# Kernel optimization log

Hardware: AMD Instinct MI355X
Metric: run time of the kernel (lower is better)

## Reference

```python
import jax, jax.numpy as jnp
import numpy as np

B, N, C = 2, 384, 128
D = C // 4          # bottleneck_dim
H = 128             # time_mlp_hidden_dim


def setup_inputs() -> dict:
    key = jax.random.key(0)
    ks = jax.random.split(key, 12)
    s = 0.02
    return {
        "edge_embed": jax.random.normal(ks[0], (B, N, N, C), jnp.float32),
        "edge_mask": jax.random.randint(ks[1], (B, N, N), 0, 2, jnp.int32),
        "r3_t": jax.random.uniform(ks[2], (B,), jnp.float32),
        # linear params stored as [in, out]
        "Wg": jax.random.normal(ks[3], (C, D), jnp.float32) * s,
        "bg": jnp.zeros((D,), jnp.float32),
        "Wv": jax.random.normal(ks[4], (C, D), jnp.float32) * s,
        "bv": jnp.zeros((D,), jnp.float32),
        "Wd": jax.random.normal(ks[5], (C, D), jnp.float32) * s,
        "bd": jnp.zeros((D,), jnp.float32),
        "Wo": jax.random.normal(ks[6], (D, C), jnp.float32) * s,
        "bo": jnp.zeros((C,), jnp.float32),
        "W1": jax.random.normal(ks[7], (1, H), jnp.float32) * s,
        "b1": jnp.zeros((H,), jnp.float32),
        "W2": jax.random.normal(ks[8], (H, 2 * C), jnp.float32) * s,
        "b2": jnp.zeros((2 * C,), jnp.float32),
    }


def reference(edge_embed, edge_mask, r3_t, Wg, bg, Wv, bv, Wd, bd, Wo, bo, W1, b1, W2, b2):
    Bb, Nn, _, Cc = edge_embed.shape
    P = edge_embed.reshape(Bb, Nn * Nn, Cc)          # [B, N^2, C]
    m = (edge_mask.reshape(Bb, Nn * Nn, 1) != 0)
    mf = m.astype(P.dtype)

    fP = P @ Wg + bg                                 # [B, N^2, D]
    gP = P @ Wv + bv                                 # [B, N^2, D]
    fP = jnp.where(m, fP, jnp.asarray(-1e8, P.dtype))
    w = jax.nn.softmax(fP, axis=1)                   # softmax over all edges
    w = w * mf
    w = w / (w.sum(axis=1, keepdims=True) + 1e-8)

    V = jnp.einsum('bnd,bne->bde', w, gP)            # [B, D, D] global context

    hP = jax.nn.softmax(P @ Wd + bd, axis=2)         # softmax over channels
    O = jnp.einsum('bnd,bde->bne', hP, V)            # redistribute
    O = (O @ Wo + bo).reshape(Bb, Nn, Nn, Cc)

    # FiLM conditioned on timestep (torch GELU is exact erf form)
    t = r3_t.reshape(Bb, 1)
    t_emb = jax.nn.gelu(t @ W1 + b1, approximate=False) @ W2 + b2
    scale, shift = jnp.split(t_emb, 2, axis=-1)
    O = O * (1 + scale[:, None, None, :]) + shift[:, None, None, :]

    return edge_embed + O
```

## Files before the change

kernel.cpp:

```cpp
#include <hip/hip_runtime.h>
#include <hip/hip_bf16.h>
#include <math.h>

#define N2 147456
#define CC 128
#define TILES 2304

#define WS_VACC 0
#define WS_S    2048
#define WS_UP   2112
#define WS_B2   10304

typedef __attribute__((ext_vector_type(8))) __bf16 bf16x8;
typedef __attribute__((ext_vector_type(4))) __bf16 bf16x4;
typedef __attribute__((ext_vector_type(4))) float f32x4;

#define MFMA16(a_, b_, c_) __builtin_amdgcn_mfma_f32_16x16x32_bf16((a_), (b_), (c_), 0, 0, 0)

__global__ void k0_zero(float* __restrict__ ws) {
    int i = blockIdx.x * 256 + threadIdx.x;
    if (i < 2112) ws[i] = 0.0f;
}

__global__ __launch_bounds__(256, 3) void k1_accum(
    const float* __restrict__ P, const int* __restrict__ mask,
    const float* __restrict__ Wg, const float* __restrict__ bg,
    const float* __restrict__ Wv, const float* __restrict__ bv,
    float* __restrict__ ws)
{
    __shared__ __bf16 ef_t[32][72];
    __shared__ __bf16 gv_t[32][72];

    const int t  = threadIdx.x;
    const int b  = blockIdx.y;
    const int w  = t >> 6;
    const int l  = t & 63;
    const int lr = l & 15;
    const int lg = l >> 4;

    bf16x8 wfrag[2][2][4];
    #pragma unroll
    for (int nt = 0; nt < 2; ++nt)
      #pragma unroll
      for (int ks = 0; ks < 4; ++ks) {
        const int base = (ks * 32 + 8 * lg) * 32 + nt * 16 + lr;
        bf16x8 f0, f1;
        #pragma unroll
        for (int i = 0; i < 8; ++i) {
            f0[i] = (__bf16)Wg[base + i * 32];
            f1[i] = (__bf16)Wv[base + i * 32];
        }
        wfrag[0][nt][ks] = f0;
        wfrag[1][nt][ks] = f1;
      }
    const float bgv[2] = { bg[lr], bg[lr + 16] };
    const float bvv[2] = { bv[lr], bv[lr + 16] };

    const int mt = w >> 1, ntq = w & 1;
    f32x4 vacc = {0.f, 0.f, 0.f, 0.f};
    float accS = 0.f;
    const int sd = t >> 3, ss = t & 7;

    const float* Pb = P + (size_t)b * N2 * CC;
    const int*   mb = mask + (size_t)b * N2;

    for (int tile = blockIdx.x; tile < TILES; tile += gridDim.x) {
        const int row0 = tile * 64 + w * 16;
        const float* prow = Pb + (size_t)(row0 + lr) * CC + 8 * lg;

        bf16x8 afrag[4];
        #pragma unroll
        for (int ks = 0; ks < 4; ++ks) {
            const float4 a0 = *(const float4*)(prow + ks * 32);
            const float4 a1 = *(const float4*)(prow + ks * 32 + 4);
            bf16x8 f;
            f[0] = (__bf16)a0.x; f[1] = (__bf16)a0.y; f[2] = (__bf16)a0.z; f[3] = (__bf16)a0.w;
            f[4] = (__bf16)a1.x; f[5] = (__bf16)a1.y; f[6] = (__bf16)a1.z; f[7] = (__bf16)a1.w;
            afrag[ks] = f;
        }

        f32x4 facc0 = {0,0,0,0}, facc1 = {0,0,0,0}, gacc0 = {0,0,0,0}, gacc1 = {0,0,0,0};
        #pragma unroll
        for (int ks = 0; ks < 4; ++ks) {
            facc0 = MFMA16(afrag[ks], wfrag[0][0][ks], facc0);
            facc1 = MFMA16(afrag[ks], wfrag[0][1][ks], facc1);
            gacc0 = MFMA16(afrag[ks], wfrag[1][0][ks], gacc0);
            gacc1 = MFMA16(afrag[ks], wfrag[1][1][ks], gacc1);
        }

        int mk[4];
        #pragma unroll
        for (int r = 0; r < 4; ++r) mk[r] = mb[row0 + lg * 4 + r];

        bf16x4 pe0, pe1, pg0, pg1;
        #pragma unroll
        for (int r = 0; r < 4; ++r) {
            pe0[r] = (__bf16)(mk[r] ? __expf(facc0[r] + bgv[0]) : 0.0f);
            pe1[r] = (__bf16)(mk[r] ? __expf(facc1[r] + bgv[1]) : 0.0f);
            pg0[r] = (__bf16)(gacc0[r] + bvv[0]);
            pg1[r] = (__bf16)(gacc1[r] + bvv[1]);
        }
        const int cbase = w * 16 + lg * 4;
        *(bf16x4*)&ef_t[lr     ][cbase] = pe0;
        *(bf16x4*)&ef_t[lr + 16][cbase] = pe1;
        *(bf16x4*)&gv_t[lr     ][cbase] = pg0;
        *(bf16x4*)&gv_t[lr + 16][cbase] = pg1;
        __syncthreads();

        #pragma unroll
        for (int ks = 0; ks < 2; ++ks) {
            const bf16x8 ea = *(const bf16x8*)&ef_t[mt  * 16 + lr][ks * 32 + 8 * lg];
            const bf16x8 gb = *(const bf16x8*)&gv_t[ntq * 16 + lr][ks * 32 + 8 * lg];
            vacc = MFMA16(ea, gb, vacc);
        }
        {
            const bf16x8 ev = *(const bf16x8*)&ef_t[sd][ss * 8];
            float s = 0.f;
            #pragma unroll
            for (int i = 0; i < 8; ++i) s += (float)ev[i];
            accS += s;
        }
        __syncthreads();
    }

    #pragma unroll
    for (int r = 0; r < 4; ++r) {
        const int d = mt * 16 + lg * 4 + r;
        const int e = ntq * 16 + lr;
        atomicAdd(ws + WS_VACC + b * 1024 + d * 32 + e, vacc[r]);
    }
    accS += __shfl_xor(accS, 1);
    accS += __shfl_xor(accS, 2);
    accS += __shfl_xor(accS, 4);
    if (ss == 0) atomicAdd(ws + WS_S + b * 32 + sd, accS);
}

__global__ __launch_bounds__(1024) void k2_finalize(
    const float* __restrict__ r3t,
    const float* __restrict__ Wo, const float* __restrict__ bo,
    const float* __restrict__ W1, const float* __restrict__ b1,
    const float* __restrict__ W2, const float* __restrict__ b2,
    float* __restrict__ ws)
{
    __shared__ float h_lds[2][128];
    __shared__ float fs_lds[2][128];
    __shared__ float sh_lds[2][128];
    __shared__ float V_lds[2048];
    __shared__ float wo_lds[32][128];
    const int t = threadIdx.x;

    ((float4*)&wo_lds[0][0])[t] = ((const float4*)Wo)[t];

    if (t < 256) {
        const int b = t >> 7, j = t & 127;
        const float x = r3t[b] * W1[j] + b1[j];
        h_lds[b][j] = 0.5f * x * (1.0f + erff(x * 0.7071067811865475f));
    }
    __syncthreads();

    if (t < 512) {
        const int b = t >> 8, j2 = t & 255;
        float acc = b2[j2];
        for (int k = 0; k < 128; ++k) acc += h_lds[b][k] * W2[k * 256 + j2];
        if (j2 < 128) fs_lds[b][j2] = 1.0f + acc;
        else          sh_lds[b][j2 - 128] = acc;
    }
    #pragma unroll
    for (int i = 0; i < 2; ++i) {
        const int idx = t + i * 1024;
        const int b = idx >> 10, d = (idx >> 5) & 31;
        const float s = ws[WS_S + b * 32 + d];
        V_lds[idx] = ws[WS_VACC + idx] / (s * (1.0f + 1e-8f));
    }
    __syncthreads();

    if (t < 256) {
        const int b = t >> 7, c = t & 127;
        ws[WS_B2 + t] = bo[c] * fs_lds[b][c] + sh_lds[b][c];
    }
    #pragma unroll
    for (int i = 0; i < 8; ++i) {
        const int idx = t + i * 1024;
        const int b = idx >> 12, d = (idx >> 7) & 31, c = idx & 127;
        float acc = 0.0f;
        #pragma unroll
        for (int e = 0; e < 32; ++e) acc += V_lds[b * 1024 + d * 32 + e] * wo_lds[e][c];
        ws[WS_UP + idx] = acc * fs_lds[b][c];
    }
}

__global__ __launch_bounds__(256, 3) void k3_out(
    const float* __restrict__ P,
    const float* __restrict__ Wd, const float* __restrict__ bd,
    const float* __restrict__ ws, float* __restrict__ out)
{
    __shared__ float  u_lds[32][132];
    __shared__ __bf16 h_t[64][40];

    const int t  = threadIdx.x;
    const int b  = blockIdx.y;
    const int w  = t >> 6, l = t & 63, lr = l & 15, lg = l >> 4;

    {
        const float4* src = (const float4*)(ws + WS_UP + b * 4096);
        const int d = t >> 3, c0 = (t & 7) * 16;
        #pragma unroll
        for (int j = 0; j < 4; ++j)
            *(float4*)&u_lds[d][c0 + 4 * j] = src[t * 4 + j];
    }

    bf16x8 wdfrag[2][4];
    #pragma unroll
    for (int nt = 0; nt < 2; ++nt)
      #pragma unroll
      for (int ks = 0; ks < 4; ++ks) {
        const int base = (ks * 32 + 8 * lg) * 32 + nt * 16 + lr;
        bf16x8 f;
        #pragma unroll
        for (int i = 0; i < 8; ++i) f[i] = (__bf16)Wd[base + i * 32];
        wdfrag[nt][ks] = f;
      }

    float bdv[8];
    #pragma unroll
    for (int r = 0; r < 4; ++r) {
        bdv[r]     = bd[lg * 4 + r];
        bdv[4 + r] = bd[16 + lg * 4 + r];
    }
    float b2v[8][4];
    #pragma unroll
    for (int nt = 0; nt < 8; ++nt) {
        const float4 v = *(const float4*)(ws + WS_B2 + b * 128 + nt * 16 + lg * 4);
        b2v[nt][0] = v.x; b2v[nt][1] = v.y; b2v[nt][2] = v.z; b2v[nt][3] = v.w;
    }

    __syncthreads();

    bf16x8 ufrag[8];
    #pragma unroll
    for (int nt = 0; nt < 8; ++nt) {
        bf16x8 f;
        #pragma unroll
        for (int i = 0; i < 8; ++i) f[i] = (__bf16)u_lds[8 * lg + i][nt * 16 + lr];
        ufrag[nt] = f;
    }

    const float* Pb = P + (size_t)b * N2 * CC;
    float*       Ob = out + (size_t)b * N2 * CC;

    for (int tile = blockIdx.x; tile < TILES; tile += gridDim.x) {
        const int row0 = tile * 64 + w * 16;
        const float* prow = Pb + (size_t)(row0 + lr) * CC + 8 * lg;

        bf16x8 afrag[4];
        #pragma unroll
        for (int ks = 0; ks < 4; ++ks) {
            const float4 a0 = *(const float4*)(prow + ks * 32);
            const float4 a1 = *(const float4*)(prow + ks * 32 + 4);
            bf16x8 f;
            f[0] = (__bf16)a0.x; f[1] = (__bf16)a0.y; f[2] = (__bf16)a0.z; f[3] = (__bf16)a0.w;
            f[4] = (__bf16)a1.x; f[5] = (__bf16)a1.y; f[6] = (__bf16)a1.z; f[7] = (__bf16)a1.w;
            afrag[ks] = f;
        }

        f32x4 dacc0 = {0,0,0,0}, dacc1 = {0,0,0,0};
        #pragma unroll
        for (int ks = 0; ks < 4; ++ks) {
            dacc0 = MFMA16(wdfrag[0][ks], afrag[ks], dacc0);
            dacc1 = MFMA16(wdfrag[1][ks], afrag[ks], dacc1);
        }

        float v[8];
        #pragma unroll
        for (int r = 0; r < 4; ++r) {
            v[r]     = dacc0[r] + bdv[r];
            v[4 + r] = dacc1[r] + bdv[4 + r];
        }
        float m = v[0];
        #pragma unroll
        for (int j = 1; j < 8; ++j) m = fmaxf(m, v[j]);
        m = fmaxf(m, __shfl_xor(m, 16));
        m = fmaxf(m, __shfl_xor(m, 32));
        float e[8], s = 0.f;
        #pragma unroll
        for (int j = 0; j < 8; ++j) { e[j] = __expf(v[j] - m); s += e[j]; }
        s += __shfl_xor(s, 16);
        s += __shfl_xor(s, 32);
        const float inv = 1.0f / s;

        bf16x4 h0, h1;
        #pragma unroll
        for (int r = 0; r < 4; ++r) {
            h0[r] = (__bf16)(e[r] * inv);
            h1[r] = (__bf16)(e[4 + r] * inv);
        }
        const int hrow = w * 16 + lr;
        *(bf16x4*)&h_t[hrow][lg * 4]      = h0;
        *(bf16x4*)&h_t[hrow][16 + lg * 4] = h1;
        const bf16x8 hf = *(const bf16x8*)&h_t[hrow][8 * lg];

        #pragma unroll
        for (int nt = 0; nt < 8; ++nt) {
            f32x4 ci;
            ci[0] = b2v[nt][0]; ci[1] = b2v[nt][1]; ci[2] = b2v[nt][2]; ci[3] = b2v[nt][3];
            const f32x4 oacc = MFMA16(ufrag[nt], hf, ci);
            const size_t off = (size_t)(row0 + lr) * CC + nt * 16 + lg * 4;
            const float4 p4 = *(const float4*)(Pb + off);
            float4 o4;
            o4.x = p4.x + oacc[0]; o4.y = p4.y + oacc[1];
            o4.z = p4.z + oacc[2]; o4.w = p4.w + oacc[3];
            *(float4*)(Ob + off) = o4;
        }
    }
}

extern "C" void kernel_launch(void* const* d_in, const int* in_sizes, int n_in,
                              void* d_out, int out_size, void* d_ws, size_t ws_size,
                              hipStream_t stream) {
    const float* P   = (const float*)d_in[0];
    const int*   msk = (const int*)d_in[1];
    const float* r3t = (const float*)d_in[2];
    const float* Wg  = (const float*)d_in[3];
    const float* bg  = (const float*)d_in[4];
    const float* Wv  = (const float*)d_in[5];
    const float* bv  = (const float*)d_in[6];
    const float* Wd  = (const float*)d_in[7];
    const float* bd  = (const float*)d_in[8];
    const float* Wo  = (const float*)d_in[9];
    const float* bo  = (const float*)d_in[10];
    const float* W1  = (const float*)d_in[11];
    const float* b1  = (const float*)d_in[12];
    const float* W2  = (const float*)d_in[13];
    const float* b2  = (const float*)d_in[14];
    float* ws  = (float*)d_ws;
    float* out = (float*)d_out;

    hipLaunchKernelGGL(k0_zero,     dim3(9),        dim3(256),  0, stream, ws);
    hipLaunchKernelGGL(k1_accum,    dim3(384, 2),   dim3(256),  0, stream, P, msk, Wg, bg, Wv, bv, ws);
    hipLaunchKernelGGL(k2_finalize, dim3(1),        dim3(1024), 0, stream, r3t, Wo, bo, W1, b1, W2, b2, ws);
    hipLaunchKernelGGL(k3_out,      dim3(768, 2),   dim3(256),  0, stream, P, Wd, bd, ws, out);
}
```

Before: 123.2 us.

## Fuse all four stages into one cooperative kernel with grid syncs

Replaces the four-kernel sequence (zero, accumulate, finalize, output) with a single cooperative launch of 768 blocks that uses grid-wide syncs between phases. Each block recomputes the small finalize step (FiLM MLP, V normalization, V·Wo) redundantly in shared memory instead of relying on a single-block kernel. The aim is to remove launch gaps and the serial one-block finalize stage. In exchange it adds grid-sync overhead, duplicated finalize work per block, and occupancy constraints, since all 768 blocks must be co-resident. It falls back to the old path if the cooperative launch fails.

```diff
diff --git a/kernel.cpp b/kernel.cpp
--- a/kernel.cpp
+++ b/kernel.cpp
@@ -1,10 +1,13 @@
 #include <hip/hip_runtime.h>
+#include <hip/hip_cooperative_groups.h>
 #include <hip/hip_bf16.h>
 #include <math.h>
 
 #define N2 147456
 #define CC 128
 #define TILES 2304
+#define HALFGRID 384
+#define GRID 768
 
 #define WS_VACC 0
 #define WS_S    2048
@@ -16,6 +19,268 @@
 typedef __attribute__((ext_vector_type(4))) float f32x4;
 
 #define MFMA16(a_, b_, c_) __builtin_amdgcn_mfma_f32_16x16x32_bf16((a_), (b_), (c_), 0, 0, 0)
+
+__global__ __launch_bounds__(256, 3) void fused_all(
+    const float* __restrict__ P, const int* __restrict__ mask,
+    const float* __restrict__ r3t,
+    const float* __restrict__ Wg, const float* __restrict__ bg,
+    const float* __restrict__ Wv, const float* __restrict__ bv,
+    const float* __restrict__ Wd, const float* __restrict__ bd,
+    const float* __restrict__ Wo, const float* __restrict__ bo,
+    const float* __restrict__ W1, const float* __restrict__ b1,
+    const float* __restrict__ W2, const float* __restrict__ b2,
+    float* __restrict__ ws, float* __restrict__ out)
+{
+    __shared__ __align__(16) __bf16 ef_t[32][72];
+    __shared__ __align__(16) __bf16 gv_t[32][72];
+    __shared__ __align__(16) float  u_lds[32][132];
+    __shared__ __align__(16) __bf16 h_t[64][40];
+    __shared__ __align__(16) float  fin_V[1024];
+    __shared__ __align__(16) float  fin_h[128];
+    __shared__ __align__(16) float  fin_fs[128];
+    __shared__ __align__(16) float  fin_b2[128];
+
+    const int t  = threadIdx.x;
+    const int bx = blockIdx.x;
+    const int b  = (bx >= HALFGRID) ? 1 : 0;
+    const int tile0 = bx - b * HALFGRID;
+    const int w  = t >> 6;
+    const int l  = t & 63;
+    const int lr = l & 15;
+    const int lg = l >> 4;
+
+    {
+        const int gid = bx * 256 + t;
+        if (gid < 2112) ws[gid] = 0.0f;
+    }
+
+    bf16x8 wfrag[2][2][4];
+    #pragma unroll
+    for (int nt = 0; nt < 2; ++nt)
+      #pragma unroll
+      for (int ks = 0; ks < 4; ++ks) {
+        const int base = (ks * 32 + 8 * lg) * 32 + nt * 16 + lr;
+        bf16x8 f0, f1;
+        #pragma unroll
+        for (int i = 0; i < 8; ++i) {
+            f0[i] = (__bf16)Wg[base + i * 32];
+            f1[i] = (__bf16)Wv[base + i * 32];
+        }
+        wfrag[0][nt][ks] = f0;
+        wfrag[1][nt][ks] = f1;
+      }
+    const float bgv[2] = { bg[lr], bg[lr + 16] };
+    const float bvv[2] = { bv[lr], bv[lr + 16] };
+
+    cooperative_groups::this_grid().sync();
+
+    const float* Pb = P + (size_t)b * N2 * CC;
+
+    {
+        const int* mb = mask + (size_t)b * N2;
+        const int mt = w >> 1, ntq = w & 1;
+        f32x4 vacc = {0.f, 0.f, 0.f, 0.f};
+        float accS = 0.f;
+        const int sd = t >> 3, ss = t & 7;
+
+        for (int tile = tile0; tile < TILES; tile += HALFGRID) {
+            const int row0 = tile * 64 + w * 16;
+            const float* prow = Pb + (size_t)(row0 + lr) * CC + 8 * lg;
+
+            bf16x8 afrag[4];
+            #pragma unroll
+            for (int ks = 0; ks < 4; ++ks) {
+                const float4 a0 = *(const float4*)(prow + ks * 32);
+                const float4 a1 = *(const float4*)(prow + ks * 32 + 4);
+                bf16x8 f;
+                f[0] = (__bf16)a0.x; f[1] = (__bf16)a0.y; f[2] = (__bf16)a0.z; f[3] = (__bf16)a0.w;
+                f[4] = (__bf16)a1.x; f[5] = (__bf16)a1.y; f[6] = (__bf16)a1.z; f[7] = (__bf16)a1.w;
+                afrag[ks] = f;
+            }
+
+            f32x4 facc0 = {0,0,0,0}, facc1 = {0,0,0,0}, gacc0 = {0,0,0,0}, gacc1 = {0,0,0,0};
+            #pragma unroll
+            for (int ks = 0; ks < 4; ++ks) {
+                facc0 = MFMA16(afrag[ks], wfrag[0][0][ks], facc0);
+                facc1 = MFMA16(afrag[ks], wfrag[0][1][ks], facc1);
+                gacc0 = MFMA16(afrag[ks], wfrag[1][0][ks], gacc0);
+                gacc1 = MFMA16(afrag[ks], wfrag[1][1][ks], gacc1);
+            }
+
+            int mk[4];
+            #pragma unroll
+            for (int r = 0; r < 4; ++r) mk[r] = mb[row0 + lg * 4 + r];
+
+            bf16x4 pe0, pe1, pg0, pg1;
+            #pragma unroll
+            for (int r = 0; r < 4; ++r) {
+                pe0[r] = (__bf16)(mk[r] ? __expf(facc0[r] + bgv[0]) : 0.0f);
+                pe1[r] = (__bf16)(mk[r] ? __expf(facc1[r] + bgv[1]) : 0.0f);
+                pg0[r] = (__bf16)(gacc0[r] + bvv[0]);
+                pg1[r] = (__bf16)(gacc1[r] + bvv[1]);
+            }
+            const int cbase = w * 16 + lg * 4;
+            *(bf16x4*)&ef_t[lr     ][cbase] = pe0;
+            *(bf16x4*)&ef_t[lr + 16][cbase] = pe1;
+            *(bf16x4*)&gv_t[lr     ][cbase] = pg0;
+            *(bf16x4*)&gv_t[lr + 16][cbase] = pg1;
+            __syncthreads();
+
+            #pragma unroll
+            for (int ks = 0; ks < 2; ++ks) {
+                const bf16x8 ea = *(const bf16x8*)&ef_t[mt  * 16 + lr][ks * 32 + 8 * lg];
+                const bf16x8 gb = *(const bf16x8*)&gv_t[ntq * 16 + lr][ks * 32 + 8 * lg];
+                vacc = MFMA16(ea, gb, vacc);
+            }
+            {
+                const bf16x8 ev = *(const bf16x8*)&ef_t[sd][ss * 8];
+                float s = 0.f;
+                #pragma unroll
+                for (int i = 0; i < 8; ++i) s += (float)ev[i];
+                accS += s;
+            }
+            __syncthreads();
+        }
+
+        #pragma unroll
+        for (int r = 0; r < 4; ++r) {
+            const int d = mt * 16 + lg * 4 + r;
+            const int e = ntq * 16 + lr;
+            atomicAdd(ws + WS_VACC + b * 1024 + d * 32 + e, vacc[r]);
+        }
+        accS += __shfl_xor(accS, 1);
+        accS += __shfl_xor(accS, 2);
+        accS += __shfl_xor(accS, 4);
+        if (ss == 0) atomicAdd(ws + WS_S + b * 32 + sd, accS);
+    }
+
+    __threadfence();
+    cooperative_groups::this_grid().sync();
+
+    {
+        if (t < 128) {
+            const float x = r3t[b] * W1[t] + b1[t];
+            fin_h[t] = 0.5f * x * (1.0f + erff(x * 0.7071067811865475f));
+        }
+        #pragma unroll
+        for (int i = 0; i < 4; ++i) {
+            const int idx = t + i * 256;
+            const int d = idx >> 5;
+            const float s = ws[WS_S + b * 32 + d];
+            fin_V[idx] = ws[WS_VACC + b * 1024 + idx] / (s * (1.0f + 1e-8f));
+        }
+        __syncthreads();
+        {
+            float acc = b2[t];
+            for (int k = 0; k < 128; ++k) acc += fin_h[k] * W2[k * 256 + t];
+            if (t < 128) fin_fs[t] = 1.0f + acc;
+            else         fin_b2[t - 128] = acc;
+        }
+        __syncthreads();
+        if (t < 128) fin_b2[t] = bo[t] * fin_fs[t] + fin_b2[t];
+        #pragma unroll
+        for (int i = 0; i < 16; ++i) {
+            const int idx = t + i * 256;
+            const int d = idx >> 7, c = idx & 127;
+            float acc = 0.0f;
+            #pragma unroll
+            for (int e = 0; e < 32; ++e) acc += fin_V[d * 32 + e] * Wo[e * 128 + c];
+            u_lds[d][c] = acc * fin_fs[c];
+        }
+        __syncthreads();
+    }
+
+    {
+        bf16x8 wdfrag[2][4];
+        #pragma unroll
+        for (int nt = 0; nt < 2; ++nt)
+          #pragma unroll
+          for (int ks = 0; ks < 4; ++ks) {
+            const int base = (ks * 32 + 8 * lg) * 32 + nt * 16 + lr;
+            bf16x8 f;
+            #pragma unroll
+            for (int i = 0; i < 8; ++i) f[i] = (__bf16)Wd[base + i * 32];
+            wdfrag[nt][ks] = f;
+          }
+        float bdv[8];
+        #pragma unroll
+        for (int r = 0; r < 4; ++r) {
+            bdv[r]     = bd[lg * 4 + r];
+            bdv[4 + r] = bd[16 + lg * 4 + r];
+        }
+        bf16x8 ufrag[8];
+        #pragma unroll
+        for (int nt = 0; nt < 8; ++nt) {
+            bf16x8 f;
+            #pragma unroll
+            for (int i = 0; i < 8; ++i) f[i] = (__bf16)u_lds[8 * lg + i][nt * 16 + lr];
+            ufrag[nt] = f;
+        }
+        float* Ob = out + (size_t)b * N2 * CC;
+
+        for (int tile = tile0; tile < TILES; tile += HALFGRID) {
+            const int row0 = tile * 64 + w * 16;
+            const float* prow = Pb + (size_t)(row0 + lr) * CC + 8 * lg;
+
+            bf16x8 afrag[4];
+            #pragma unroll
+            for (int ks = 0; ks < 4; ++ks) {
+                const float4 a0 = *(const float4*)(prow + ks * 32);
+                const float4 a1 = *(const float4*)(prow + ks * 32 + 4);
+                bf16x8 f;
+                f[0] = (__bf16)a0.x; f[1] = (__bf16)a0.y; f[2] = (__bf16)a0.z; f[3] = (__bf16)a0.w;
+                f[4] = (__bf16)a1.x; f[5] = (__bf16)a1.y; f[6] = (__bf16)a1.z; f[7] = (__bf16)a1.w;
+                afrag[ks] = f;
+            }
+
+            f32x4 dacc0 = {0,0,0,0}, dacc1 = {0,0,0,0};
+            #pragma unroll
+            for (int ks = 0; ks < 4; ++ks) {
+                dacc0 = MFMA16(wdfrag[0][ks], afrag[ks], dacc0);
+                dacc1 = MFMA16(wdfrag[1][ks], afrag[ks], dacc1);
+            }
+
+            float v[8];
+            #pragma unroll
+            for (int r = 0; r < 4; ++r) {
+                v[r]     = dacc0[r] + bdv[r];
+                v[4 + r] = dacc1[r] + bdv[4 + r];
+            }
+            float m = v[0];
+            #pragma unroll
+            for (int j = 1; j < 8; ++j) m = fmaxf(m, v[j]);
+            m = fmaxf(m, __shfl_xor(m, 16));
+            m = fmaxf(m, __shfl_xor(m, 32));
+            float e[8], s = 0.f;
+            #pragma unroll
+            for (int j = 0; j < 8; ++j) { e[j] = __expf(v[j] - m); s += e[j]; }
+            s += __shfl_xor(s, 16);
+            s += __shfl_xor(s, 32);
+            const float inv = 1.0f / s;
+
+            bf16x4 h0, h1;
+            #pragma unroll
+            for (int r = 0; r < 4; ++r) {
+                h0[r] = (__bf16)(e[r] * inv);
+                h1[r] = (__bf16)(e[4 + r] * inv);
+            }
+            const int hrow = w * 16 + lr;
+            *(bf16x4*)&h_t[hrow][lg * 4]      = h0;
+            *(bf16x4*)&h_t[hrow][16 + lg * 4] = h1;
+            const bf16x8 hf = *(const bf16x8*)&h_t[hrow][8 * lg];
+
+            #pragma unroll
+            for (int nt = 0; nt < 8; ++nt) {
+                const f32x4 ci = *(const f32x4*)&fin_b2[nt * 16 + lg * 4];
+                const f32x4 oacc = MFMA16(ufrag[nt], hf, ci);
+                const size_t off = (size_t)(row0 + lr) * CC + nt * 16 + lg * 4;
+                const f32x4 p4 = *(const f32x4*)(Pb + off);
+                const f32x4 o4 = p4 + oacc;
+                __builtin_nontemporal_store(o4, (f32x4*)(Ob + off));
+            }
+        }
+    }
+}
 
 __global__ void k0_zero(float* __restrict__ ws) {
     int i = blockIdx.x * 256 + threadIdx.x;
@@ -335,8 +600,20 @@
     float* ws  = (float*)d_ws;
     float* out = (float*)d_out;
 
-    hipLaunchKernelGGL(k0_zero,     dim3(9),        dim3(256),  0, stream, ws);
-    hipLaunchKernelGGL(k1_accum,    dim3(384, 2),   dim3(256),  0, stream, P, msk, Wg, bg, Wv, bv, ws);
-    hipLaunchKernelGGL(k2_finalize, dim3(1),        dim3(1024), 0, stream, r3t, Wo, bo, W1, b1, W2, b2, ws);
-    hipLaunchKernelGGL(k3_out,      dim3(768, 2),   dim3(256),  0, stream, P, Wd, bd, ws, out);
+    void* args[] = {
+        (void*)&P,  (void*)&msk, (void*)&r3t,
+        (void*)&Wg, (void*)&bg,  (void*)&Wv, (void*)&bv,
+        (void*)&Wd, (void*)&bd,  (void*)&Wo, (void*)&bo,
+        (void*)&W1, (void*)&b1,  (void*)&W2, (void*)&b2,
+        (void*)&ws, (void*)&out };
+
+    hipError_t err = hipLaunchCooperativeKernel(
+        reinterpret_cast<void*>(fused_all), dim3(GRID), dim3(256), args, 0, stream);
+
+    if (err != hipSuccess) {
+        hipLaunchKernelGGL(k0_zero,     dim3(9),        dim3(256),  0, stream, ws);
+        hipLaunchKernelGGL(k1_accum,    dim3(384, 2),   dim3(256),  0, stream, P, msk, Wg, bg, Wv, bv, ws);
+        hipLaunchKernelGGL(k2_finalize, dim3(1),        dim3(1024), 0, stream, r3t, Wo, bo, W1, b1, W2, b2, ws);
+        hipLaunchKernelGGL(k3_out,      dim3(768, 2),   dim3(256),  0, stream, P, Wd, bd, ws, out);
+    }
 }
```

Measured after the change: 331.5 us. 2.69x slower.

## Fold finalize kernel into init and output kernels, reverse tile order

Applied to the files above, without the earlier changes.

Removes the single-block finalize kernel. The timestep MLP moves into the zeroing kernel, and every output block now recomputes V normalization and V@Wo into shared memory itself. This drops one serial launch and its single-block latency, at the cost of redundant per-block compute (32x32x128 MACs with global Wo reads) in each of the 1536 output blocks. Mask loads become a vectorized int4 load, and output tiles are traversed in reverse so recently cached rows of P from the accumulate pass may be reused.

```diff
diff --git a/kernel.cpp b/kernel.cpp
--- a/kernel.cpp
+++ b/kernel.cpp
@@ -8,8 +8,8 @@
 
 #define WS_VACC 0
 #define WS_S    2048
-#define WS_UP   2112
-#define WS_B2   10304
+#define WS_FS   2112
+#define WS_SH   2368
 
 typedef __attribute__((ext_vector_type(8))) __bf16 bf16x8;
 typedef __attribute__((ext_vector_type(4))) __bf16 bf16x4;
@@ -17,9 +17,39 @@
 
 #define MFMA16(a_, b_, c_) __builtin_amdgcn_mfma_f32_16x16x32_bf16((a_), (b_), (c_), 0, 0, 0)
 
-__global__ void k0_zero(float* __restrict__ ws) {
-    int i = blockIdx.x * 256 + threadIdx.x;
-    if (i < 2112) ws[i] = 0.0f;
+__global__ __launch_bounds__(256) void k0_init(
+    const float* __restrict__ r3t,
+    const float* __restrict__ W1, const float* __restrict__ b1,
+    const float* __restrict__ W2, const float* __restrict__ b2,
+    float* __restrict__ ws)
+{
+    const int t = threadIdx.x, bx = blockIdx.x;
+    if (bx > 0) {
+        const int i = (bx - 1) * 256 + t;
+        if (i < 2112) ws[i] = 0.0f;
+        return;
+    }
+    __shared__ float h[2][128];
+    {
+        const int b = t >> 7, j = t & 127;
+        const float x = r3t[b] * W1[j] + b1[j];
+        h[b][j] = 0.5f * x * (1.0f + erff(x * 0.7071067811865475f));
+    }
+    __syncthreads();
+    const int j2 = t;
+    float acc0 = b2[j2], acc1 = b2[j2];
+    for (int k = 0; k < 128; ++k) {
+        const float w2 = W2[k * 256 + j2];
+        acc0 += h[0][k] * w2;
+        acc1 += h[1][k] * w2;
+    }
+    if (j2 < 128) {
+        ws[WS_FS + j2]       = 1.0f + acc0;
+        ws[WS_FS + 128 + j2] = 1.0f + acc1;
+    } else {
+        ws[WS_SH + (j2 - 128)]       = acc0;
+        ws[WS_SH + 128 + (j2 - 128)] = acc1;
+    }
 }
 
 __global__ __launch_bounds__(256, 3) void k1_accum(
@@ -88,9 +118,8 @@
             gacc1 = MFMA16(afrag[ks], wfrag[1][1][ks], gacc1);
         }
 
-        int mk[4];
-        #pragma unroll
-        for (int r = 0; r < 4; ++r) mk[r] = mb[row0 + lg * 4 + r];
+        const int4 mk4 = *(const int4*)&mb[row0 + lg * 4];
+        const int mk[4] = { mk4.x, mk4.y, mk4.z, mk4.w };
 
         bf16x4 pe0, pe1, pg0, pg1;
         #pragma unroll
@@ -135,78 +164,33 @@
     if (ss == 0) atomicAdd(ws + WS_S + b * 32 + sd, accS);
 }
 
-__global__ __launch_bounds__(1024) void k2_finalize(
-    const float* __restrict__ r3t,
-    const float* __restrict__ Wo, const float* __restrict__ bo,
-    const float* __restrict__ W1, const float* __restrict__ b1,
-    const float* __restrict__ W2, const float* __restrict__ b2,
-    float* __restrict__ ws)
-{
-    __shared__ float h_lds[2][128];
-    __shared__ float fs_lds[2][128];
-    __shared__ float sh_lds[2][128];
-    __shared__ float V_lds[2048];
-    __shared__ float wo_lds[32][128];
-    const int t = threadIdx.x;
-
-    ((float4*)&wo_lds[0][0])[t] = ((const float4*)Wo)[t];
-
-    if (t < 256) {
-        const int b = t >> 7, j = t & 127;
-        const float x = r3t[b] * W1[j] + b1[j];
-        h_lds[b][j] = 0.5f * x * (1.0f + erff(x * 0.7071067811865475f));
-    }
-    __syncthreads();
-
-    if (t < 512) {
-        const int b = t >> 8, j2 = t & 255;
-        float acc = b2[j2];
-        for (int k = 0; k < 128; ++k) acc += h_lds[b][k] * W2[k * 256 + j2];
-        if (j2 < 128) fs_lds[b][j2] = 1.0f + acc;
-        else          sh_lds[b][j2 - 128] = acc;
-    }
-    #pragma unroll
-    for (int i = 0; i < 2; ++i) {
-        const int idx = t + i * 1024;
-        const int b = idx >> 10, d = (idx >> 5) & 31;
-        const float s = ws[WS_S + b * 32 + d];
-        V_lds[idx] = ws[WS_VACC + idx] / (s * (1.0f + 1e-8f));
-    }
-    __syncthreads();
-
-    if (t < 256) {
-        const int b = t >> 7, c = t & 127;
-        ws[WS_B2 + t] = bo[c] * fs_lds[b][c] + sh_lds[b][c];
-    }
-    #pragma unroll
-    for (int i = 0; i < 8; ++i) {
-        const int idx = t + i * 1024;
-        const int b = idx >> 12, d = (idx >> 7) & 31, c = idx & 127;
-        float acc = 0.0f;
-        #pragma unroll
-        for (int e = 0; e < 32; ++e) acc += V_lds[b * 1024 + d * 32 + e] * wo_lds[e][c];
-        ws[WS_UP + idx] = acc * fs_lds[b][c];
-    }
-}
-
 __global__ __launch_bounds__(256, 3) void k3_out(
     const float* __restrict__ P,
     const float* __restrict__ Wd, const float* __restrict__ bd,
+    const float* __restrict__ Wo, const float* __restrict__ bo,
     const float* __restrict__ ws, float* __restrict__ out)
 {
     __shared__ float  u_lds[32][132];
     __shared__ __bf16 h_t[64][40];
+    __shared__ float  fin_V[1024];
+    __shared__ float  fin_fs[128];
+    __shared__ float  fin_b2[128];
 
     const int t  = threadIdx.x;
     const int b  = blockIdx.y;
     const int w  = t >> 6, l = t & 63, lr = l & 15, lg = l >> 4;
 
-    {
-        const float4* src = (const float4*)(ws + WS_UP + b * 4096);
-        const int d = t >> 3, c0 = (t & 7) * 16;
-        #pragma unroll
-        for (int j = 0; j < 4; ++j)
-            *(float4*)&u_lds[d][c0 + 4 * j] = src[t * 4 + j];
+    if (t < 128) {
+        const float fs = ws[WS_FS + b * 128 + t];
+        fin_fs[t] = fs;
+        fin_b2[t] = bo[t] * fs + ws[WS_SH + b * 128 + t];
+    }
+    #pragma unroll
+    for (int i = 0; i < 4; ++i) {
+        const int idx = t + i * 256;
+        const int d = idx >> 5;
+        const float s = ws[WS_S + b * 32 + d];
+        fin_V[idx] = ws[WS_VACC + b * 1024 + idx] / (s * (1.0f + 1e-8f));
     }
 
     bf16x8 wdfrag[2][4];
@@ -220,20 +204,24 @@
         for (int i = 0; i < 8; ++i) f[i] = (__bf16)Wd[base + i * 32];
         wdfrag[nt][ks] = f;
       }
-
     float bdv[8];
     #pragma unroll
     for (int r = 0; r < 4; ++r) {
         bdv[r]     = bd[lg * 4 + r];
         bdv[4 + r] = bd[16 + lg * 4 + r];
     }
-    float b2v[8][4];
-    #pragma unroll
-    for (int nt = 0; nt < 8; ++nt) {
-        const float4 v = *(const float4*)(ws + WS_B2 + b * 128 + nt * 16 + lg * 4);
-        b2v[nt][0] = v.x; b2v[nt][1] = v.y; b2v[nt][2] = v.z; b2v[nt][3] = v.w;
-    }
-
+
+    __syncthreads();
+
+    #pragma unroll
+    for (int i = 0; i < 16; ++i) {
+        const int idx = t + i * 256;
+        const int d = idx >> 7, c = idx & 127;
+        float acc = 0.0f;
+        #pragma unroll
+        for (int e = 0; e < 32; ++e) acc += fin_V[d * 32 + e] * Wo[e * 128 + c];
+        u_lds[d][c] = acc * fin_fs[c];
+    }
     __syncthreads();
 
     bf16x8 ufrag[8];
@@ -244,11 +232,17 @@
         for (int i = 0; i < 8; ++i) f[i] = (__bf16)u_lds[8 * lg + i][nt * 16 + lr];
         ufrag[nt] = f;
     }
+    float b2v[8][4];
+    #pragma unroll
+    for (int nt = 0; nt < 8; ++nt) {
+        const float4 v = *(const float4*)&fin_b2[nt * 16 + lg * 4];
+        b2v[nt][0] = v.x; b2v[nt][1] = v.y; b2v[nt][2] = v.z; b2v[nt][3] = v.w;
+    }
 
     const float* Pb = P + (size_t)b * N2 * CC;
     float*       Ob = out + (size_t)b * N2 * CC;
 
-    for (int tile = blockIdx.x; tile < TILES; tile += gridDim.x) {
+    for (int tile = TILES - 1 - blockIdx.x; tile >= 0; tile -= gridDim.x) {
         const int row0 = tile * 64 + w * 16;
         const float* prow = Pb + (size_t)(row0 + lr) * CC + 8 * lg;
 
@@ -335,8 +329,7 @@
     float* ws  = (float*)d_ws;
     float* out = (float*)d_out;
 
-    hipLaunchKernelGGL(k0_zero,     dim3(9),        dim3(256),  0, stream, ws);
-    hipLaunchKernelGGL(k1_accum,    dim3(384, 2),   dim3(256),  0, stream, P, msk, Wg, bg, Wv, bv, ws);
-    hipLaunchKernelGGL(k2_finalize, dim3(1),        dim3(1024), 0, stream, r3t, Wo, bo, W1, b1, W2, b2, ws);
-    hipLaunchKernelGGL(k3_out,      dim3(768, 2),   dim3(256),  0, stream, P, Wd, bd, ws, out);
+    hipLaunchKernelGGL(k0_init,  dim3(10),      dim3(256), 0, stream, r3t, W1, b1, W2, b2, ws);
+    hipLaunchKernelGGL(k1_accum, dim3(384, 2),  dim3(256), 0, stream, P, msk, Wg, bg, Wv, bv, ws);
+    hipLaunchKernelGGL(k3_out,   dim3(768, 2),  dim3(256), 0, stream, P, Wd, bd, Wo, bo, ws, out);
 }
```

Result: slower. 133.8 us (+8.6%).
